# Optimization experiments

Measured on AMD Instinct MI355X. Metric: run time of the kernel, lower is better.

The kernel has to match this reference:

```python
import jax, jax.numpy as jnp
import numpy as np

N_TEMPS = 6
OUT_SIZE = 4     # estimated temperatures (state size)
N_NONTEMP = 5    # electrical input features
SAMPLE_TIME = 0.5


def _adjacency():
    # maps node pair (i, j) -> conductance index in the upper-triangular flat layout
    adj = np.zeros((N_TEMPS, N_TEMPS), dtype=np.int32)
    iu = np.triu_indices(N_TEMPS, 1)
    adj[iu] = np.arange(len(iu[0]), dtype=np.int32)  # cumsum(ones)-1
    adj += adj.T
    return adj


def setup_inputs() -> dict:
    key = jax.random.key(0)
    ks = jax.random.split(key, 8)
    B, T, F = 4096, 512, N_NONTEMP + 2
    n_conds = N_TEMPS * (N_TEMPS - 1) // 2  # 15
    inputs = jax.random.normal(ks[0], (B, T, F), dtype=jnp.float32)
    # caps initializer: RandomNormal(mean=-3, stddev=0.5)
    caps = -3.0 + 0.5 * jax.random.normal(ks[1], (1, OUT_SIZE), dtype=jnp.float32)
    Wg = jax.random.normal(ks[2], (11, n_conds), dtype=jnp.float32) * 0.3
    bg = jnp.zeros((n_conds,), dtype=jnp.float32)
    Wp1 = jax.random.normal(ks[3], (11, 16), dtype=jnp.float32) * 0.3
    bp1 = jnp.zeros((16,), dtype=jnp.float32)
    Wp2 = jax.random.normal(ks[4], (16, OUT_SIZE), dtype=jnp.float32) * 0.3
    bp2 = jnp.zeros((OUT_SIZE,), dtype=jnp.float32)
    return {"inputs": inputs, "caps": caps, "Wg": Wg, "bg": bg,
            "Wp1": Wp1, "bp1": bp1, "Wp2": Wp2, "bp2": bp2}


def reference(inputs, caps, Wg, bg, Wp1, bp1, Wp2, bp2):
    B = inputs.shape[0]
    adj = _adjacency()
    A = jnp.asarray(adj[:OUT_SIZE, :])                          # [4, 6] conductance gather idx
    mask = np.ones((OUT_SIZE, N_TEMPS), dtype=np.float32)
    mask[np.arange(OUT_SIZE), np.arange(OUT_SIZE)] = 0.0        # exclude j == i
    mask = jnp.asarray(mask)
    inv_caps = 10.0 ** caps                                     # [1, 4]

    def step(prev, x):
        temps = jnp.concatenate([prev, x[:, N_NONTEMP:]], axis=1)     # [B, 6]
        all_in = jnp.concatenate([x[:, :N_NONTEMP], temps], axis=1)   # [B, 11]
        conducts = jax.nn.sigmoid(all_in @ Wg + bg)                   # [B, 15]
        cg = conducts[:, A]                                           # [B, 4, 6]
        d = temps[:, None, :] - prev[:, :, None]                      # [B, 4, 6]
        temp_diffs = jnp.sum(d * cg * mask, axis=-1)                  # [B, 4]
        ploss = jnp.abs(jnp.tanh(all_in @ Wp1 + bp1) @ Wp2 + bp2)     # [B, 4]
        new = jnp.clip(prev + SAMPLE_TIME * inv_caps * (temp_diffs + ploss), -1.0, 5.0)
        return new, prev  # keras cell emits prev_out as per-step output

    init = jnp.zeros((B, OUT_SIZE), dtype=inputs.dtype)
    _, outs = jax.lax.scan(step, init, jnp.swapaxes(inputs, 0, 1))
    return jnp.swapaxes(outs, 0, 1)  # [B, T, 4]
```

## Files before the change

### kernel.cpp

```cpp
#include <hip/hip_runtime.h>


template <int CTRL>
__device__ __forceinline__ float dppadd(float v) {
  int x = __builtin_amdgcn_update_dpp(0, __float_as_int(v), CTRL, 0xF, 0xF, true);
  return v + __int_as_float(x);
}
#define DPP_XOR1 0xB1
#define DPP_XOR2 0x4E
#define DPP_ROR4 0x124
#define DPP_ROR8 0x128

__global__ __launch_bounds__(64, 1) void tnn_scan(
    const float* __restrict__ in,
    const float* __restrict__ caps,
    const float* __restrict__ Wg,
    const float* __restrict__ bg,
    const float* __restrict__ Wp1,
    const float* __restrict__ bp1,
    const float* __restrict__ Wp2,
    const float* __restrict__ bp2,
    float* __restrict__ out)
{
  __shared__ float xb[2][4][449];

  const int lane = threadIdx.x;
  const int grp  = lane >> 4;
  const int u    = lane & 15;
  const int ur   = u & 3;

  const int elem = (int)blockIdx.x * 4 + grp;

  const int ug = (u < 15) ? u : 14;
  const float wg0 = Wg[0*15+ug], wg1 = Wg[1*15+ug], wg2 = Wg[2*15+ug],
              wg3 = Wg[3*15+ug], wg4 = Wg[4*15+ug], wg5 = Wg[5*15+ug],
              wg6 = Wg[6*15+ug], wg7 = Wg[7*15+ug], wg8 = Wg[8*15+ug],
              wg9 = Wg[9*15+ug], wg10 = Wg[10*15+ug];
  const float bgc = bg[ug];
  const float wp0 = Wp1[0*16+u], wp1 = Wp1[1*16+u], wp2 = Wp1[2*16+u],
              wp3 = Wp1[3*16+u], wp4 = Wp1[4*16+u], wp5 = Wp1[5*16+u],
              wp6 = Wp1[6*16+u], wp7 = Wp1[7*16+u], wp8 = Wp1[8*16+u],
              wp9 = Wp1[9*16+u], wp10 = Wp1[10*16+u];
  const float bhc = bp1[u];
  const float w20 = Wp2[u*4+0], w21 = Wp2[u*4+1], w22 = Wp2[u*4+2], w23 = Wp2[u*4+3];

  const float b20 = bp2[0], b21 = bp2[1], b22 = bp2[2], b23 = bp2[3];
  const float LN10 = 2.302585092994046f;
  const float kc0 = 0.5f * __expf(caps[0] * LN10);
  const float kc1 = 0.5f * __expf(caps[1] * LN10);
  const float kc2 = 0.5f * __expf(caps[2] * LN10);
  const float kc3 = 0.5f * __expf(caps[3] * LN10);

  const unsigned long long IPACK = 0x4433222111100000ULL;
  const unsigned long long JPACK = 0x5554543543254321ULL;
  const int pi = (int)((IPACK >> (4 * u)) & 15);
  const int pj = (int)((JPACK >> (4 * u)) & 15);
  const float is0 = (pi == 0) ? 1.f : 0.f, is1 = (pi == 1) ? 1.f : 0.f,
              is2 = (pi == 2) ? 1.f : 0.f, is3 = (pi == 3) ? 1.f : 0.f;
  const float tj1 = (pj == 1) ? 1.f : 0.f, tj2 = (pj == 2) ? 1.f : 0.f,
              tj3 = (pj == 3) ? 1.f : 0.f, tj4 = (pj == 4) ? 1.f : 0.f,
              tj5 = (pj == 5) ? 1.f : 0.f;

  float s0 = 0.f, s1 = 0.f, s2 = 0.f, s3 = 0.f;

  const float* inblk = in + (size_t)((int)blockIdx.x * 4) * 3584;
  float* op = out + (size_t)elem * 2048 + ur;

  float stg[4][7];
  auto LOADC = [&](int cc) {
    #pragma unroll
    for (int e = 0; e < 4; ++e)
      #pragma unroll
      for (int k = 0; k < 7; ++k)
        stg[e][k] = inblk[(size_t)e * 3584 + cc * 448 + k * 64 + lane];
  };
  auto WRITEC = [&](int bb) {
    #pragma unroll
    for (int e = 0; e < 4; ++e)
      #pragma unroll
      for (int k = 0; k < 7; ++k)
        xb[bb][e][k * 64 + lane] = stg[e][k];
  };

  LOADC(0);
  WRITEC(0);

  #pragma unroll 1
  for (int c = 0; c < 8; ++c) {
    if (c < 7) LOADC(c + 1);
    const int cb = c & 1;

    #pragma unroll 4
    for (int tin = 0; tin < 64; ++tin) {
      const int t = c * 64 + tin;
      const float* xr = &xb[cb][grp][tin * 7];
      const float x0 = xr[0], x1 = xr[1], x2 = xr[2], x3 = xr[3],
                  x4 = xr[4], x5 = xr[5], x6 = xr[6];

      float zgx = fmaf(x0, wg0, fmaf(x1, wg1, fmaf(x2, wg2, fmaf(x3, wg3,
                  fmaf(x4, wg4, fmaf(x5, wg9, fmaf(x6, wg10, bgc)))))));
      float zhx = fmaf(x0, wp0, fmaf(x1, wp1, fmaf(x2, wp2, fmaf(x3, wp3,
                  fmaf(x4, wp4, fmaf(x5, wp9, fmaf(x6, wp10, bhc)))))));
      float txx = fmaf(tj4, x5, tj5 * x6);

      const float zg = fmaf(s0, wg5, fmaf(s1, wg6, fmaf(s2, wg7, fmaf(s3, wg8, zgx))));
      const float zh = fmaf(s0, wp5, fmaf(s1, wp6, fmaf(s2, wp7, fmaf(s3, wp8, zhx))));

      const float g = __fdividef(1.0f, 1.0f + __expf(-zg));
      const float h = 1.0f - 2.0f * __fdividef(1.0f, 1.0f + __expf(2.0f * zh));

      float p0 = h * w20, p1 = h * w21, p2 = h * w22, p3 = h * w23;

      const float sjp = fmaf(tj1, s1, fmaf(tj2, s2, tj3 * s3));
      const float Si  = fmaf(is0, s0, fmaf(is1, s1, fmaf(is2, s2, is3 * s3)));
      const float Tj  = sjp + txx;
      const float ci  = g * (Tj - Si);
      const float cj  = g * (Si - sjp);
      float t0 = is0 * ci;
      float t1 = fmaf(is1, ci, tj1 * cj);
      float t2 = fmaf(is2, ci, tj2 * cj);
      float t3 = fmaf(is3, ci, tj3 * cj);

      p0 = dppadd<DPP_XOR1>(p0); p1 = dppadd<DPP_XOR1>(p1);
      p2 = dppadd<DPP_XOR1>(p2); p3 = dppadd<DPP_XOR1>(p3);
      t0 = dppadd<DPP_XOR1>(t0); t1 = dppadd<DPP_XOR1>(t1);
      t2 = dppadd<DPP_XOR1>(t2); t3 = dppadd<DPP_XOR1>(t3);
      p0 = dppadd<DPP_XOR2>(p0); p1 = dppadd<DPP_XOR2>(p1);
      p2 = dppadd<DPP_XOR2>(p2); p3 = dppadd<DPP_XOR2>(p3);
      t0 = dppadd<DPP_XOR2>(t0); t1 = dppadd<DPP_XOR2>(t1);
      t2 = dppadd<DPP_XOR2>(t2); t3 = dppadd<DPP_XOR2>(t3);
      p0 = dppadd<DPP_ROR4>(p0); p1 = dppadd<DPP_ROR4>(p1);
      p2 = dppadd<DPP_ROR4>(p2); p3 = dppadd<DPP_ROR4>(p3);
      t0 = dppadd<DPP_ROR4>(t0); t1 = dppadd<DPP_ROR4>(t1);
      t2 = dppadd<DPP_ROR4>(t2); t3 = dppadd<DPP_ROR4>(t3);
      p0 = dppadd<DPP_ROR8>(p0); p1 = dppadd<DPP_ROR8>(p1);
      p2 = dppadd<DPP_ROR8>(p2); p3 = dppadd<DPP_ROR8>(p3);
      t0 = dppadd<DPP_ROR8>(t0); t1 = dppadd<DPP_ROR8>(t1);
      t2 = dppadd<DPP_ROR8>(t2); t3 = dppadd<DPP_ROR8>(t3);

      const float sout = (ur == 0) ? s0 : (ur == 1) ? s1 : (ur == 2) ? s2 : s3;
      if (u < 4) op[t * 4] = sout;

      const float pl0 = fabsf(p0 + b20);
      const float pl1 = fabsf(p1 + b21);
      const float pl2 = fabsf(p2 + b22);
      const float pl3 = fabsf(p3 + b23);
      s0 = fminf(fmaxf(fmaf(kc0, t0 + pl0, s0), -1.0f), 5.0f);
      s1 = fminf(fmaxf(fmaf(kc1, t1 + pl1, s1), -1.0f), 5.0f);
      s2 = fminf(fmaxf(fmaf(kc2, t2 + pl2, s2), -1.0f), 5.0f);
      s3 = fminf(fmaxf(fmaf(kc3, t3 + pl3, s3), -1.0f), 5.0f);
    }

    if (c < 7) WRITEC((c + 1) & 1);
  }
}

extern "C" void kernel_launch(void* const* d_in, const int* in_sizes, int n_in,
                              void* d_out, int out_size, void* d_ws, size_t ws_size,
                              hipStream_t stream) {
  const float* in   = (const float*)d_in[0];
  const float* caps = (const float*)d_in[1];
  const float* Wg   = (const float*)d_in[2];
  const float* bg   = (const float*)d_in[3];
  const float* Wp1  = (const float*)d_in[4];
  const float* bp1  = (const float*)d_in[5];
  const float* Wp2  = (const float*)d_in[6];
  const float* bp2  = (const float*)d_in[7];
  float* out = (float*)d_out;

  hipLaunchKernelGGL(tnn_scan, dim3(1024), dim3(64), 0, stream,
                     in, caps, Wg, bg, Wp1, bp1, Wp2, bp2, out);
}
```

Before: 271.5 us.

## Split sigmoid and tanh branches across wave halves, two chains per wave

Each 64-lane wave now handles two batch chains instead of four. The lower 32 lanes compute the conductance sigmoid path and the upper 32 lanes compute the tanh power-loss path, with lane-dependent constants selecting which branch each lane runs. The two halves are combined with a permlane32 swap, which halves the per-lane exp/divide and DPP-reduction work on the serial recurrence. The grid doubles, launch bounds allow two waves per SIMD, and the clamp uses med3. The cost is more waves and redundant same-value stores from lanes whose u is 4 or more.

```diff
diff --git a/kernel.cpp b/kernel.cpp
--- a/kernel.cpp
+++ b/kernel.cpp
@@ -11,7 +11,13 @@
 #define DPP_ROR4 0x124
 #define DPP_ROR8 0x128
 
-__global__ __launch_bounds__(64, 1) void tnn_scan(
+__device__ __forceinline__ float other_half(float v) {
+  unsigned b = __float_as_uint(v);
+  auto sw = __builtin_amdgcn_permlane32_swap(b, b, false, false);
+  return __uint_as_float(b ^ sw[0] ^ sw[1]);
+}
+
+__global__ __launch_bounds__(64, 2) void tnn_scan(
     const float* __restrict__ in,
     const float* __restrict__ caps,
     const float* __restrict__ Wg,
@@ -22,61 +28,77 @@
     const float* __restrict__ bp2,
     float* __restrict__ out)
 {
-  __shared__ float xb[2][4][449];
+  __shared__ float xb[2][2][449];
 
-  const int lane = threadIdx.x;
-  const int grp  = lane >> 4;
-  const int u    = lane & 15;
-  const int ur   = u & 3;
+  const int lane  = threadIdx.x;
+  const int chain = (lane >> 4) & 1;
+  const int u     = lane & 15;
+  const bool hB   = (lane >= 32);
+  const int ur    = u & 3;
 
-  const int elem = (int)blockIdx.x * 4 + grp;
+  const int elem = (int)blockIdx.x * 2 + chain;
 
   const int ug = (u < 15) ? u : 14;
-  const float wg0 = Wg[0*15+ug], wg1 = Wg[1*15+ug], wg2 = Wg[2*15+ug],
-              wg3 = Wg[3*15+ug], wg4 = Wg[4*15+ug], wg5 = Wg[5*15+ug],
-              wg6 = Wg[6*15+ug], wg7 = Wg[7*15+ug], wg8 = Wg[8*15+ug],
-              wg9 = Wg[9*15+ug], wg10 = Wg[10*15+ug];
-  const float bgc = bg[ug];
-  const float wp0 = Wp1[0*16+u], wp1 = Wp1[1*16+u], wp2 = Wp1[2*16+u],
-              wp3 = Wp1[3*16+u], wp4 = Wp1[4*16+u], wp5 = Wp1[5*16+u],
-              wp6 = Wp1[6*16+u], wp7 = Wp1[7*16+u], wp8 = Wp1[8*16+u],
-              wp9 = Wp1[9*16+u], wp10 = Wp1[10*16+u];
-  const float bhc = bp1[u];
-  const float w20 = Wp2[u*4+0], w21 = Wp2[u*4+1], w22 = Wp2[u*4+2], w23 = Wp2[u*4+3];
+  const unsigned long long IPACK = 0x4433222111100000ULL;
+  const unsigned long long JPACK = 0x5554543543254321ULL;
+  const int pi = (int)((IPACK >> (4 * ug)) & 15);
+  const int pj = (int)((JPACK >> (4 * ug)) & 15);
 
-  const float b20 = bp2[0], b21 = bp2[1], b22 = bp2[2], b23 = bp2[3];
+  float wv0, wv1, wv2, wv3, wv4, wv5, wv6, wv7, wv8, wv9, wv10, bias;
+  float mexp, cA, cB;
+  float w20, w21, w22, w23;
+  float is0, is1, is2, is3, tj1, tj2, tj3, tj4, tj5;
+  if (!hB) {
+    wv0 = Wg[0*15+ug]; wv1 = Wg[1*15+ug]; wv2 = Wg[2*15+ug];
+    wv3 = Wg[3*15+ug]; wv4 = Wg[4*15+ug]; wv5 = Wg[5*15+ug];
+    wv6 = Wg[6*15+ug]; wv7 = Wg[7*15+ug]; wv8 = Wg[8*15+ug];
+    wv9 = Wg[9*15+ug]; wv10 = Wg[10*15+ug]; bias = bg[ug];
+    mexp = -1.0f; cA = 1.0f; cB = 0.0f;
+    w20 = w21 = w22 = w23 = 0.0f;
+    is0 = (pi == 0) ? 1.f : 0.f; is1 = (pi == 1) ? 1.f : 0.f;
+    is2 = (pi == 2) ? 1.f : 0.f; is3 = (pi == 3) ? 1.f : 0.f;
+    tj1 = (pj == 1) ? 1.f : 0.f; tj2 = (pj == 2) ? 1.f : 0.f;
+    tj3 = (pj == 3) ? 1.f : 0.f; tj4 = (pj == 4) ? 1.f : 0.f;
+    tj5 = (pj == 5) ? 1.f : 0.f;
+  } else {
+    wv0 = Wp1[0*16+u]; wv1 = Wp1[1*16+u]; wv2 = Wp1[2*16+u];
+    wv3 = Wp1[3*16+u]; wv4 = Wp1[4*16+u]; wv5 = Wp1[5*16+u];
+    wv6 = Wp1[6*16+u]; wv7 = Wp1[7*16+u]; wv8 = Wp1[8*16+u];
+    wv9 = Wp1[9*16+u]; wv10 = Wp1[10*16+u]; bias = bp1[u];
+    mexp = 2.0f; cA = -2.0f; cB = 1.0f;
+    w20 = Wp2[u*4+0]; w21 = Wp2[u*4+1]; w22 = Wp2[u*4+2]; w23 = Wp2[u*4+3];
+    is0 = is1 = is2 = is3 = 0.f;
+    tj1 = tj2 = tj3 = tj4 = tj5 = 0.f;
+  }
+
+  const float B0 = hB ? bp2[0] : 0.0f;
+  const float B1 = hB ? bp2[1] : 0.0f;
+  const float B2 = hB ? bp2[2] : 0.0f;
+  const float B3 = hB ? bp2[3] : 0.0f;
+  const unsigned MABS = hB ? 0x7FFFFFFFu : 0xFFFFFFFFu;
+
   const float LN10 = 2.302585092994046f;
   const float kc0 = 0.5f * __expf(caps[0] * LN10);
   const float kc1 = 0.5f * __expf(caps[1] * LN10);
   const float kc2 = 0.5f * __expf(caps[2] * LN10);
   const float kc3 = 0.5f * __expf(caps[3] * LN10);
 
-  const unsigned long long IPACK = 0x4433222111100000ULL;
-  const unsigned long long JPACK = 0x5554543543254321ULL;
-  const int pi = (int)((IPACK >> (4 * u)) & 15);
-  const int pj = (int)((JPACK >> (4 * u)) & 15);
-  const float is0 = (pi == 0) ? 1.f : 0.f, is1 = (pi == 1) ? 1.f : 0.f,
-              is2 = (pi == 2) ? 1.f : 0.f, is3 = (pi == 3) ? 1.f : 0.f;
-  const float tj1 = (pj == 1) ? 1.f : 0.f, tj2 = (pj == 2) ? 1.f : 0.f,
-              tj3 = (pj == 3) ? 1.f : 0.f, tj4 = (pj == 4) ? 1.f : 0.f,
-              tj5 = (pj == 5) ? 1.f : 0.f;
-
   float s0 = 0.f, s1 = 0.f, s2 = 0.f, s3 = 0.f;
 
-  const float* inblk = in + (size_t)((int)blockIdx.x * 4) * 3584;
+  const float* inblk = in + (size_t)((int)blockIdx.x * 2) * 3584;
   float* op = out + (size_t)elem * 2048 + ur;
 
-  float stg[4][7];
+  float stg[2][7];
   auto LOADC = [&](int cc) {
     #pragma unroll
-    for (int e = 0; e < 4; ++e)
+    for (int e = 0; e < 2; ++e)
       #pragma unroll
       for (int k = 0; k < 7; ++k)
         stg[e][k] = inblk[(size_t)e * 3584 + cc * 448 + k * 64 + lane];
   };
   auto WRITEC = [&](int bb) {
     #pragma unroll
-    for (int e = 0; e < 4; ++e)
+    for (int e = 0; e < 2; ++e)
       #pragma unroll
       for (int k = 0; k < 7; ++k)
         xb[bb][e][k * 64 + lane] = stg[e][k];
@@ -93,62 +115,58 @@
     #pragma unroll 4
     for (int tin = 0; tin < 64; ++tin) {
       const int t = c * 64 + tin;
-      const float* xr = &xb[cb][grp][tin * 7];
+      const float* xr = &xb[cb][chain][tin * 7];
       const float x0 = xr[0], x1 = xr[1], x2 = xr[2], x3 = xr[3],
                   x4 = xr[4], x5 = xr[5], x6 = xr[6];
 
-      float zgx = fmaf(x0, wg0, fmaf(x1, wg1, fmaf(x2, wg2, fmaf(x3, wg3,
-                  fmaf(x4, wg4, fmaf(x5, wg9, fmaf(x6, wg10, bgc)))))));
-      float zhx = fmaf(x0, wp0, fmaf(x1, wp1, fmaf(x2, wp2, fmaf(x3, wp3,
-                  fmaf(x4, wp4, fmaf(x5, wp9, fmaf(x6, wp10, bhc)))))));
-      float txx = fmaf(tj4, x5, tj5 * x6);
+      float z = fmaf(x0, wv0, fmaf(x1, wv1, fmaf(x2, wv2, fmaf(x3, wv3,
+                fmaf(x4, wv4, fmaf(x5, wv9, fmaf(x6, wv10, bias)))))));
+      z = fmaf(s0, wv5, fmaf(s1, wv6, fmaf(s2, wv7, fmaf(s3, wv8, z))));
 
-      const float zg = fmaf(s0, wg5, fmaf(s1, wg6, fmaf(s2, wg7, fmaf(s3, wg8, zgx))));
-      const float zh = fmaf(s0, wp5, fmaf(s1, wp6, fmaf(s2, wp7, fmaf(s3, wp8, zhx))));
+      const float e1 = __expf(z * mexp);
+      const float rr = __fdividef(1.0f, 1.0f + e1);
+      const float val = fmaf(rr, cA, cB);
 
-      const float g = __fdividef(1.0f, 1.0f + __expf(-zg));
-      const float h = 1.0f - 2.0f * __fdividef(1.0f, 1.0f + __expf(2.0f * zh));
-
-      float p0 = h * w20, p1 = h * w21, p2 = h * w22, p3 = h * w23;
-
+      const float txx = fmaf(tj4, x5, tj5 * x6);
       const float sjp = fmaf(tj1, s1, fmaf(tj2, s2, tj3 * s3));
       const float Si  = fmaf(is0, s0, fmaf(is1, s1, fmaf(is2, s2, is3 * s3)));
+      const float gS  = val * Si;
       const float Tj  = sjp + txx;
-      const float ci  = g * (Tj - Si);
-      const float cj  = g * (Si - sjp);
-      float t0 = is0 * ci;
-      float t1 = fmaf(is1, ci, tj1 * cj);
-      float t2 = fmaf(is2, ci, tj2 * cj);
-      float t3 = fmaf(is3, ci, tj3 * cj);
+      const float ci  = fmaf(val, Tj, -gS);
+      const float cj  = fmaf(-val, sjp, gS);
 
-      p0 = dppadd<DPP_XOR1>(p0); p1 = dppadd<DPP_XOR1>(p1);
-      p2 = dppadd<DPP_XOR1>(p2); p3 = dppadd<DPP_XOR1>(p3);
-      t0 = dppadd<DPP_XOR1>(t0); t1 = dppadd<DPP_XOR1>(t1);
-      t2 = dppadd<DPP_XOR1>(t2); t3 = dppadd<DPP_XOR1>(t3);
-      p0 = dppadd<DPP_XOR2>(p0); p1 = dppadd<DPP_XOR2>(p1);
-      p2 = dppadd<DPP_XOR2>(p2); p3 = dppadd<DPP_XOR2>(p3);
-      t0 = dppadd<DPP_XOR2>(t0); t1 = dppadd<DPP_XOR2>(t1);
-      t2 = dppadd<DPP_XOR2>(t2); t3 = dppadd<DPP_XOR2>(t3);
-      p0 = dppadd<DPP_ROR4>(p0); p1 = dppadd<DPP_ROR4>(p1);
-      p2 = dppadd<DPP_ROR4>(p2); p3 = dppadd<DPP_ROR4>(p3);
-      t0 = dppadd<DPP_ROR4>(t0); t1 = dppadd<DPP_ROR4>(t1);
-      t2 = dppadd<DPP_ROR4>(t2); t3 = dppadd<DPP_ROR4>(t3);
-      p0 = dppadd<DPP_ROR8>(p0); p1 = dppadd<DPP_ROR8>(p1);
-      p2 = dppadd<DPP_ROR8>(p2); p3 = dppadd<DPP_ROR8>(p3);
-      t0 = dppadd<DPP_ROR8>(t0); t1 = dppadd<DPP_ROR8>(t1);
-      t2 = dppadd<DPP_ROR8>(t2); t3 = dppadd<DPP_ROR8>(t3);
+      float v0 = fmaf(val, w20, is0 * ci);
+      float v1 = fmaf(val, w21, fmaf(is1, ci, tj1 * cj));
+      float v2 = fmaf(val, w22, fmaf(is2, ci, tj2 * cj));
+      float v3 = fmaf(val, w23, fmaf(is3, ci, tj3 * cj));
 
-      const float sout = (ur == 0) ? s0 : (ur == 1) ? s1 : (ur == 2) ? s2 : s3;
-      if (u < 4) op[t * 4] = sout;
+      v0 = dppadd<DPP_XOR1>(v0); v1 = dppadd<DPP_XOR1>(v1);
+      v2 = dppadd<DPP_XOR1>(v2); v3 = dppadd<DPP_XOR1>(v3);
+      v0 = dppadd<DPP_XOR2>(v0); v1 = dppadd<DPP_XOR2>(v1);
+      v2 = dppadd<DPP_XOR2>(v2); v3 = dppadd<DPP_XOR2>(v3);
+      v0 = dppadd<DPP_ROR4>(v0); v1 = dppadd<DPP_ROR4>(v1);
+      v2 = dppadd<DPP_ROR4>(v2); v3 = dppadd<DPP_ROR4>(v3);
+      v0 = dppadd<DPP_ROR8>(v0); v1 = dppadd<DPP_ROR8>(v1);
+      v2 = dppadd<DPP_ROR8>(v2); v3 = dppadd<DPP_ROR8>(v3);
 
-      const float pl0 = fabsf(p0 + b20);
-      const float pl1 = fabsf(p1 + b21);
-      const float pl2 = fabsf(p2 + b22);
-      const float pl3 = fabsf(p3 + b23);
-      s0 = fminf(fmaxf(fmaf(kc0, t0 + pl0, s0), -1.0f), 5.0f);
-      s1 = fminf(fmaxf(fmaf(kc1, t1 + pl1, s1), -1.0f), 5.0f);
-      s2 = fminf(fmaxf(fmaf(kc2, t2 + pl2, s2), -1.0f), 5.0f);
-      s3 = fminf(fmaxf(fmaf(kc3, t3 + pl3, s3), -1.0f), 5.0f);
+      const float o0 = __uint_as_float(__float_as_uint(v0 + B0) & MABS);
+      const float o1 = __uint_as_float(__float_as_uint(v1 + B1) & MABS);
+      const float o2 = __uint_as_float(__float_as_uint(v2 + B2) & MABS);
+      const float o3 = __uint_as_float(__float_as_uint(v3 + B3) & MABS);
+
+      const float u0 = o0 + other_half(o0);
+      const float u1 = o1 + other_half(o1);
+      const float u2 = o2 + other_half(o2);
+      const float u3 = o3 + other_half(o3);
+
+      const float sa = (ur & 1) ? s1 : s0;
+      const float sb = (ur & 1) ? s3 : s2;
+      op[t * 4] = (ur & 2) ? sb : sa;
+
+      s0 = __builtin_amdgcn_fmed3f(fmaf(kc0, u0, s0), -1.0f, 5.0f);
+      s1 = __builtin_amdgcn_fmed3f(fmaf(kc1, u1, s1), -1.0f, 5.0f);
+      s2 = __builtin_amdgcn_fmed3f(fmaf(kc2, u2, s2), -1.0f, 5.0f);
+      s3 = __builtin_amdgcn_fmed3f(fmaf(kc3, u3, s3), -1.0f, 5.0f);
     }
 
     if (c < 7) WRITEC((c + 1) & 1);
@@ -168,6 +186,6 @@
   const float* bp2  = (const float*)d_in[7];
   float* out = (float*)d_out;
 
-  hipLaunchKernelGGL(tnn_scan, dim3(1024), dim3(64), 0, stream,
+  hipLaunchKernelGGL(tnn_scan, dim3(2048), dim3(64), 0, stream,
                      in, caps, Wg, bg, Wp1, bp1, Wp2, bp2, out);
 }
```

Result: slower. 303.3 us (+11.7%).

## Shorten per-step dependency chain with folded constants, split FMA trees and fused DPP adds

Applied to the files above, without the earlier changes.

Pre-scales the gate and hidden weights by -log2(e) and 2*log2(e) so the sigmoid and tanh become raw exp2 plus rcp. The dot products are split into two parallel FMA chains to shorten the serial latency, and the bp2 bias is folded into one lane before the reduction. The reductions use inline-asm v_add_f32 with a DPP modifier instead of a separate update_dpp plus add, and the clamp uses med3. All of this targets the latency of the serial recurrence, at the cost of approximate exp/rcp accuracy and inline asm that hides DPP hazards from the compiler.

```diff
diff --git a/kernel.cpp b/kernel.cpp
--- a/kernel.cpp
+++ b/kernel.cpp
@@ -1,15 +1,30 @@
 #include <hip/hip_runtime.h>
 
 
-template <int CTRL>
-__device__ __forceinline__ float dppadd(float v) {
-  int x = __builtin_amdgcn_update_dpp(0, __float_as_int(v), CTRL, 0xF, 0xF, true);
-  return v + __int_as_float(x);
+__device__ __forceinline__ float dpp_xor1(float v) {
+  float r;
+  asm("v_add_f32 %0, %1, %2 quad_perm:[1,0,3,2] row_mask:0xf bank_mask:0xf"
+      : "=v"(r) : "v"(v), "v"(v));
+  return r;
 }
-#define DPP_XOR1 0xB1
-#define DPP_XOR2 0x4E
-#define DPP_ROR4 0x124
-#define DPP_ROR8 0x128
+__device__ __forceinline__ float dpp_xor2(float v) {
+  float r;
+  asm("v_add_f32 %0, %1, %2 quad_perm:[2,3,0,1] row_mask:0xf bank_mask:0xf"
+      : "=v"(r) : "v"(v), "v"(v));
+  return r;
+}
+__device__ __forceinline__ float dpp_ror4(float v) {
+  float r;
+  asm("v_add_f32 %0, %1, %2 row_ror:4 row_mask:0xf bank_mask:0xf"
+      : "=v"(r) : "v"(v), "v"(v));
+  return r;
+}
+__device__ __forceinline__ float dpp_ror8(float v) {
+  float r;
+  asm("v_add_f32 %0, %1, %2 row_ror:8 row_mask:0xf bank_mask:0xf"
+      : "=v"(r) : "v"(v), "v"(v));
+  return r;
+}
 
 __global__ __launch_bounds__(64, 1) void tnn_scan(
     const float* __restrict__ in,
@@ -31,20 +46,27 @@
 
   const int elem = (int)blockIdx.x * 4 + grp;
 
+  const float L  = 1.4426950408889634f;
+  const float SG = -L, TH = 2.0f * L;
+
   const int ug = (u < 15) ? u : 14;
-  const float wg0 = Wg[0*15+ug], wg1 = Wg[1*15+ug], wg2 = Wg[2*15+ug],
-              wg3 = Wg[3*15+ug], wg4 = Wg[4*15+ug], wg5 = Wg[5*15+ug],
-              wg6 = Wg[6*15+ug], wg7 = Wg[7*15+ug], wg8 = Wg[8*15+ug],
-              wg9 = Wg[9*15+ug], wg10 = Wg[10*15+ug];
-  const float bgc = bg[ug];
-  const float wp0 = Wp1[0*16+u], wp1 = Wp1[1*16+u], wp2 = Wp1[2*16+u],
-              wp3 = Wp1[3*16+u], wp4 = Wp1[4*16+u], wp5 = Wp1[5*16+u],
-              wp6 = Wp1[6*16+u], wp7 = Wp1[7*16+u], wp8 = Wp1[8*16+u],
-              wp9 = Wp1[9*16+u], wp10 = Wp1[10*16+u];
-  const float bhc = bp1[u];
+  const float wg0 = Wg[0*15+ug]*SG, wg1 = Wg[1*15+ug]*SG, wg2 = Wg[2*15+ug]*SG,
+              wg3 = Wg[3*15+ug]*SG, wg4 = Wg[4*15+ug]*SG, wg5 = Wg[5*15+ug]*SG,
+              wg6 = Wg[6*15+ug]*SG, wg7 = Wg[7*15+ug]*SG, wg8 = Wg[8*15+ug]*SG,
+              wg9 = Wg[9*15+ug]*SG, wg10 = Wg[10*15+ug]*SG;
+  const float bgc = bg[ug]*SG;
+  const float wp0 = Wp1[0*16+u]*TH, wp1 = Wp1[1*16+u]*TH, wp2 = Wp1[2*16+u]*TH,
+              wp3 = Wp1[3*16+u]*TH, wp4 = Wp1[4*16+u]*TH, wp5 = Wp1[5*16+u]*TH,
+              wp6 = Wp1[6*16+u]*TH, wp7 = Wp1[7*16+u]*TH, wp8 = Wp1[8*16+u]*TH,
+              wp9 = Wp1[9*16+u]*TH, wp10 = Wp1[10*16+u]*TH;
+  const float bhc = bp1[u]*TH;
   const float w20 = Wp2[u*4+0], w21 = Wp2[u*4+1], w22 = Wp2[u*4+2], w23 = Wp2[u*4+3];
 
-  const float b20 = bp2[0], b21 = bp2[1], b22 = bp2[2], b23 = bp2[3];
+  const float bb0 = (u == 15) ? bp2[0] : 0.f;
+  const float bb1 = (u == 15) ? bp2[1] : 0.f;
+  const float bb2 = (u == 15) ? bp2[2] : 0.f;
+  const float bb3 = (u == 15) ? bp2[3] : 0.f;
+
   const float LN10 = 2.302585092994046f;
   const float kc0 = 0.5f * __expf(caps[0] * LN10);
   const float kc1 = 0.5f * __expf(caps[1] * LN10);
@@ -53,8 +75,8 @@
 
   const unsigned long long IPACK = 0x4433222111100000ULL;
   const unsigned long long JPACK = 0x5554543543254321ULL;
-  const int pi = (int)((IPACK >> (4 * u)) & 15);
-  const int pj = (int)((JPACK >> (4 * u)) & 15);
+  const int pi = (int)((IPACK >> (4 * ug)) & 15);
+  const int pj = (int)((JPACK >> (4 * ug)) & 15);
   const float is0 = (pi == 0) ? 1.f : 0.f, is1 = (pi == 1) ? 1.f : 0.f,
               is2 = (pi == 2) ? 1.f : 0.f, is3 = (pi == 3) ? 1.f : 0.f;
   const float tj1 = (pj == 1) ? 1.f : 0.f, tj2 = (pj == 2) ? 1.f : 0.f,
@@ -97,58 +119,56 @@
       const float x0 = xr[0], x1 = xr[1], x2 = xr[2], x3 = xr[3],
                   x4 = xr[4], x5 = xr[5], x6 = xr[6];
 
-      float zgx = fmaf(x0, wg0, fmaf(x1, wg1, fmaf(x2, wg2, fmaf(x3, wg3,
-                  fmaf(x4, wg4, fmaf(x5, wg9, fmaf(x6, wg10, bgc)))))));
-      float zhx = fmaf(x0, wp0, fmaf(x1, wp1, fmaf(x2, wp2, fmaf(x3, wp3,
-                  fmaf(x4, wp4, fmaf(x5, wp9, fmaf(x6, wp10, bhc)))))));
-      float txx = fmaf(tj4, x5, tj5 * x6);
+      float zgA = fmaf(x0, wg0, fmaf(x2, wg2, fmaf(x4, wg4,
+                  fmaf(s1, wg6, fmaf(s3, wg8, fmaf(x6, wg10, bgc))))));
+      float zgB = fmaf(x1, wg1, fmaf(x3, wg3, fmaf(s0, wg5,
+                  fmaf(s2, wg7, x5 * wg9))));
+      float zhA = fmaf(x0, wp0, fmaf(x2, wp2, fmaf(x4, wp4,
+                  fmaf(s1, wp6, fmaf(s3, wp8, fmaf(x6, wp10, bhc))))));
+      float zhB = fmaf(x1, wp1, fmaf(x3, wp3, fmaf(s0, wp5,
+                  fmaf(s2, wp7, x5 * wp9))));
+      const float zg = zgA + zgB;
+      const float zh = zhA + zhB;
 
-      const float zg = fmaf(s0, wg5, fmaf(s1, wg6, fmaf(s2, wg7, fmaf(s3, wg8, zgx))));
-      const float zh = fmaf(s0, wp5, fmaf(s1, wp6, fmaf(s2, wp7, fmaf(s3, wp8, zhx))));
+      const float g = __builtin_amdgcn_rcpf(1.0f + __builtin_amdgcn_exp2f(zg));
+      const float rh = __builtin_amdgcn_rcpf(1.0f + __builtin_amdgcn_exp2f(zh));
+      const float h = fmaf(rh, -2.0f, 1.0f);
 
-      const float g = __fdividef(1.0f, 1.0f + __expf(-zg));
-      const float h = 1.0f - 2.0f * __fdividef(1.0f, 1.0f + __expf(2.0f * zh));
+      float p0 = fmaf(h, w20, bb0), p1 = fmaf(h, w21, bb1),
+            p2 = fmaf(h, w22, bb2), p3 = fmaf(h, w23, bb3);
 
-      float p0 = h * w20, p1 = h * w21, p2 = h * w22, p3 = h * w23;
-
+      const float txx = fmaf(tj4, x5, tj5 * x6);
       const float sjp = fmaf(tj1, s1, fmaf(tj2, s2, tj3 * s3));
       const float Si  = fmaf(is0, s0, fmaf(is1, s1, fmaf(is2, s2, is3 * s3)));
-      const float Tj  = sjp + txx;
-      const float ci  = g * (Tj - Si);
-      const float cj  = g * (Si - sjp);
+      const float d   = Si - sjp;
+      const float gd  = g * d;
+      const float ci  = fmaf(g, txx, -gd);
+      const float cj  = gd;
       float t0 = is0 * ci;
       float t1 = fmaf(is1, ci, tj1 * cj);
       float t2 = fmaf(is2, ci, tj2 * cj);
       float t3 = fmaf(is3, ci, tj3 * cj);
 
-      p0 = dppadd<DPP_XOR1>(p0); p1 = dppadd<DPP_XOR1>(p1);
-      p2 = dppadd<DPP_XOR1>(p2); p3 = dppadd<DPP_XOR1>(p3);
-      t0 = dppadd<DPP_XOR1>(t0); t1 = dppadd<DPP_XOR1>(t1);
-      t2 = dppadd<DPP_XOR1>(t2); t3 = dppadd<DPP_XOR1>(t3);
-      p0 = dppadd<DPP_XOR2>(p0); p1 = dppadd<DPP_XOR2>(p1);
-      p2 = dppadd<DPP_XOR2>(p2); p3 = dppadd<DPP_XOR2>(p3);
-      t0 = dppadd<DPP_XOR2>(t0); t1 = dppadd<DPP_XOR2>(t1);
-      t2 = dppadd<DPP_XOR2>(t2); t3 = dppadd<DPP_XOR2>(t3);
-      p0 = dppadd<DPP_ROR4>(p0); p1 = dppadd<DPP_ROR4>(p1);
-      p2 = dppadd<DPP_ROR4>(p2); p3 = dppadd<DPP_ROR4>(p3);
-      t0 = dppadd<DPP_ROR4>(t0); t1 = dppadd<DPP_ROR4>(t1);
-      t2 = dppadd<DPP_ROR4>(t2); t3 = dppadd<DPP_ROR4>(t3);
-      p0 = dppadd<DPP_ROR8>(p0); p1 = dppadd<DPP_ROR8>(p1);
-      p2 = dppadd<DPP_ROR8>(p2); p3 = dppadd<DPP_ROR8>(p3);
-      t0 = dppadd<DPP_ROR8>(t0); t1 = dppadd<DPP_ROR8>(t1);
-      t2 = dppadd<DPP_ROR8>(t2); t3 = dppadd<DPP_ROR8>(t3);
+      p0 = dpp_xor1(p0); p1 = dpp_xor1(p1); p2 = dpp_xor1(p2); p3 = dpp_xor1(p3);
+      t0 = dpp_xor1(t0); t1 = dpp_xor1(t1); t2 = dpp_xor1(t2); t3 = dpp_xor1(t3);
+      p0 = dpp_xor2(p0); p1 = dpp_xor2(p1); p2 = dpp_xor2(p2); p3 = dpp_xor2(p3);
+      t0 = dpp_xor2(t0); t1 = dpp_xor2(t1); t2 = dpp_xor2(t2); t3 = dpp_xor2(t3);
+      p0 = dpp_ror4(p0); p1 = dpp_ror4(p1); p2 = dpp_ror4(p2); p3 = dpp_ror4(p3);
+      t0 = dpp_ror4(t0); t1 = dpp_ror4(t1); t2 = dpp_ror4(t2); t3 = dpp_ror4(t3);
+      p0 = dpp_ror8(p0); p1 = dpp_ror8(p1); p2 = dpp_ror8(p2); p3 = dpp_ror8(p3);
+      t0 = dpp_ror8(t0); t1 = dpp_ror8(t1); t2 = dpp_ror8(t2); t3 = dpp_ror8(t3);
 
       const float sout = (ur == 0) ? s0 : (ur == 1) ? s1 : (ur == 2) ? s2 : s3;
       if (u < 4) op[t * 4] = sout;
 
-      const float pl0 = fabsf(p0 + b20);
-      const float pl1 = fabsf(p1 + b21);
-      const float pl2 = fabsf(p2 + b22);
-      const float pl3 = fabsf(p3 + b23);
-      s0 = fminf(fmaxf(fmaf(kc0, t0 + pl0, s0), -1.0f), 5.0f);
-      s1 = fminf(fmaxf(fmaf(kc1, t1 + pl1, s1), -1.0f), 5.0f);
-      s2 = fminf(fmaxf(fmaf(kc2, t2 + pl2, s2), -1.0f), 5.0f);
-      s3 = fminf(fmaxf(fmaf(kc3, t3 + pl3, s3), -1.0f), 5.0f);
+      const float u0 = t0 + fabsf(p0);
+      const float u1 = t1 + fabsf(p1);
+      const float u2 = t2 + fabsf(p2);
+      const float u3 = t3 + fabsf(p3);
+      s0 = __builtin_amdgcn_fmed3f(fmaf(kc0, u0, s0), -1.0f, 5.0f);
+      s1 = __builtin_amdgcn_fmed3f(fmaf(kc1, u1, s1), -1.0f, 5.0f);
+      s2 = __builtin_amdgcn_fmed3f(fmaf(kc2, u2, s2), -1.0f, 5.0f);
+      s3 = __builtin_amdgcn_fmed3f(fmaf(kc3, u3, s3), -1.0f, 5.0f);
     }
 
     if (c < 7) WRITEC((c + 1) & 1);
```

New measurement: 233.9 us. 13.9% less time.
